# Performance work log

Hardware: AMD Instinct MI355X
Metric: run time of the kernel (lower is better)

## Reference

```python
import jax, jax.numpy as jnp
import numpy as np

EPS = 1e-7


def setup_inputs() -> dict:
    key = jax.random.key(0)
    k1, k2, k3, k4 = jax.random.split(key, 4)
    S, N, R, CIN, COUT = 16, 1024, 4, 128, 128
    A = jax.random.uniform(k1, (S, N, N, R + 1), dtype=jnp.float32)
    x = jax.random.normal(k2, (S, N, CIN), dtype=jnp.float32)
    weight = jax.random.normal(k3, (CIN, COUT, R), dtype=jnp.float32) * 0.02
    theta_root = jax.random.normal(k4, (CIN, COUT), dtype=jnp.float32) * 0.02
    return {"A": A, "x": x, "weight": weight, "theta_root": theta_root}


def reference(A, x, weight, theta_root):
    # Drop the last relation channel ('no-edge' type in MolGAN)
    Ar = A[..., :-1]                                   # (s, N, N, R)
    # Per-destination, per-relation degree normalization
    norm = 1.0 / (jnp.sum(Ar, axis=2) + EPS)           # (s, N, R)
    # Fused contraction: avoid materializing Theta_ij (s,N,N,in,out).
    # x_new[s,i,b] = sum_{j,c,a} A[s,i,j,c] * norm[s,i,c] * x[s,j,a] * W[a,b,c]
    m = jnp.einsum('sijc,sja->sica', Ar, x)            # (s, N, R, in)
    m = m * norm[..., None]                            # apply norm over (s,i,c)
    agg = jnp.einsum('sica,abc->sib', m, weight)       # (s, N, out)
    x_new = agg + x @ theta_root                       # root/self term
    return jnp.tanh(x_new)
```

## Files before the change

kernel.cpp:

```cpp
#include <hip/hip_runtime.h>
#include <hip/hip_bf16.h>
#include <math.h>

#define SS    16
#define NN    1024
#define RR    4
#define CINC  128
#define COUTC 128
#define RP1   5
#define EPSF  1e-7f

typedef __bf16 bf16x8 __attribute__((ext_vector_type(8)));
typedef __bf16 bf16x4 __attribute__((ext_vector_type(4)));
typedef float  f32x4  __attribute__((ext_vector_type(4)));

#define YT_BYTES ((size_t)SS * RR * COUTC * NN * 2)

__global__ __launch_bounds__(256) void convert_kernel(
    const float* __restrict__ weight, const float* __restrict__ theta,
    __bf16* __restrict__ wT)
{
    const int idx = blockIdx.x * 256 + threadIdx.x;
    const int a = idx >> 7, b = idx & 127;
    f32x4 wv = *(const f32x4*)(weight + ((size_t)a * COUTC + b) * RR);
    wT[(0 * COUTC + b) * CINC + a] = (__bf16)wv.x;
    wT[(1 * COUTC + b) * CINC + a] = (__bf16)wv.y;
    wT[(2 * COUTC + b) * CINC + a] = (__bf16)wv.z;
    wT[(3 * COUTC + b) * CINC + a] = (__bf16)wv.w;
    wT[(4 * COUTC + b) * CINC + a] = (__bf16)theta[(size_t)a * COUTC + b];
}

__global__ __launch_bounds__(256) void prep_kernel(
    const float* __restrict__ x, const __bf16* __restrict__ wT,
    __bf16* __restrict__ Yt)
{
    const int bx = blockIdx.x;
    const int s  = bx & 15;
    const int r  = bx >> 4;
    const int ch = r & 3;
    const int jt = r >> 2;

    const int t = threadIdx.x, lane = t & 63, w = t >> 6;
    const int m16 = lane & 15, quad = lane >> 4;

    const float*  xrow = x  + ((size_t)(s * NN) + jt * 64 + w * 16 + m16) * CINC;
    const __bf16* wch  = wT + (size_t)ch * COUTC * CINC;

    f32x4 acc[8];
#pragma unroll
    for (int i = 0; i < 8; ++i) acc[i] = (f32x4){0.f, 0.f, 0.f, 0.f};

#pragma unroll
    for (int k0 = 0; k0 < CINC; k0 += 32) {
        f32x4 xa = *(const f32x4*)(xrow + k0 + quad * 8);
        f32x4 xc = *(const f32x4*)(xrow + k0 + quad * 8 + 4);
        bf16x8 af;
        af[0] = (__bf16)xa.x; af[1] = (__bf16)xa.y; af[2] = (__bf16)xa.z; af[3] = (__bf16)xa.w;
        af[4] = (__bf16)xc.x; af[5] = (__bf16)xc.y; af[6] = (__bf16)xc.z; af[7] = (__bf16)xc.w;
#pragma unroll
        for (int bs = 0; bs < 8; ++bs) {
            const bf16x8 bf = *(const bf16x8*)(wch + (size_t)(bs * 16 + m16) * CINC + k0 + quad * 8);
            acc[bs] = __builtin_amdgcn_mfma_f32_16x16x32_bf16(af, bf, acc[bs], 0, 0, 0);
        }
    }

    const int j0 = jt * 64 + w * 16 + quad * 4;
#pragma unroll
    for (int bs = 0; bs < 8; ++bs) {
        const int b = bs * 16 + m16;
        bf16x4 v; v[0] = (__bf16)acc[bs][0]; v[1] = (__bf16)acc[bs][1];
                  v[2] = (__bf16)acc[bs][2]; v[3] = (__bf16)acc[bs][3];
        *(bf16x4*)(Yt + ((size_t)((s * 4 + ch) * COUTC + b)) * NN + j0) = v;
    }
}

__global__ __launch_bounds__(256, 4) void main_kernel(
    const float* __restrict__ A, const float* __restrict__ x,
    const __bf16* __restrict__ Yt, const __bf16* __restrict__ wT,
    float* __restrict__ out)
{
    const int bx = blockIdx.x;
    const int s  = bx & 15;
    const int i0 = (bx >> 4) * 16;

    __shared__ __bf16 lA[2][4][16][72];
    __shared__ float  lnorm[4][16];

    const int t = threadIdx.x;
    const int lane = t & 63, w = t >> 6;
    const int m16 = lane & 15, quad = lane >> 4;

    const int irow = t >> 4;
    const int q    = t & 15;

    const float* Ap = A + ((size_t)(s * NN + i0 + irow) * NN) * RP1 + q * 20;

    f32x4 accz[2];
    accz[0] = (f32x4){0.f, 0.f, 0.f, 0.f};
    accz[1] = (f32x4){0.f, 0.f, 0.f, 0.f};
    {
        const float*  xrow = x  + ((size_t)(s * NN) + i0 + m16) * CINC;
        const __bf16* wth  = wT + (size_t)4 * COUTC * CINC;
#pragma unroll
        for (int k0 = 0; k0 < CINC; k0 += 32) {
            f32x4 xa = *(const f32x4*)(xrow + k0 + quad * 8);
            f32x4 xc = *(const f32x4*)(xrow + k0 + quad * 8 + 4);
            bf16x8 af;
            af[0] = (__bf16)xa.x; af[1] = (__bf16)xa.y; af[2] = (__bf16)xa.z; af[3] = (__bf16)xa.w;
            af[4] = (__bf16)xc.x; af[5] = (__bf16)xc.y; af[6] = (__bf16)xc.z; af[7] = (__bf16)xc.w;
#pragma unroll
            for (int bs = 0; bs < 2; ++bs) {
                const bf16x8 bf = *(const bf16x8*)(wth + (size_t)(w * 32 + bs * 16 + m16) * CINC + k0 + quad * 8);
                accz[bs] = __builtin_amdgcn_mfma_f32_16x16x32_bf16(af, bf, accz[bs], 0, 0, 0);
            }
        }
    }

    float rs[4] = {0.f, 0.f, 0.f, 0.f};
    f32x4 acc[4][2];
#pragma unroll
    for (int c = 0; c < 4; ++c)
#pragma unroll
        for (int bs = 0; bs < 2; ++bs) acc[c][bs] = (f32x4){0.f, 0.f, 0.f, 0.f};

    const __bf16* Ys = Yt + (size_t)s * 4 * COUTC * NN;

    f32x4 ld[5];
#pragma unroll
    for (int u = 0; u < 5; ++u) ld[u] = __builtin_nontemporal_load((const f32x4*)Ap + u);

    for (int kk = 0; kk < 16; ++kk) {
        const int p = kk & 1;

        {
            const float v0[4] = {ld[0].x, ld[1].y, ld[2].z, ld[3].w};
            const float v1[4] = {ld[0].y, ld[1].z, ld[2].w, ld[4].x};
            const float v2[4] = {ld[0].z, ld[1].w, ld[3].x, ld[4].y};
            const float v3[4] = {ld[0].w, ld[2].x, ld[3].y, ld[4].z};
            const float* vv[4] = {v0, v1, v2, v3};
#pragma unroll
            for (int c = 0; c < 4; ++c) {
                const float* v = vv[c];
                rs[c] += v[0] + v[1] + v[2] + v[3];
                bf16x4 pk; pk[0] = (__bf16)v[0]; pk[1] = (__bf16)v[1];
                           pk[2] = (__bf16)v[2]; pk[3] = (__bf16)v[3];
                *(bf16x4*)&lA[p][c][irow][q * 4] = pk;
            }
        }
        __syncthreads();

        if (kk < 15) {
            Ap += 320;
#pragma unroll
            for (int u = 0; u < 5; ++u) ld[u] = __builtin_nontemporal_load((const f32x4*)Ap + u);
        }

#pragma unroll
        for (int c = 0; c < 4; ++c) {
            const __bf16* yp = Ys + (size_t)(c * COUTC + w * 32 + m16) * NN + kk * 64 + quad * 8;
#pragma unroll
            for (int ks = 0; ks < 2; ++ks) {
                const bf16x8 af = *(const bf16x8*)&lA[p][c][m16][ks * 32 + quad * 8];
                const bf16x8 b0 = *(const bf16x8*)(yp + ks * 32);
                const bf16x8 b1 = *(const bf16x8*)(yp + (size_t)16 * NN + ks * 32);
                acc[c][0] = __builtin_amdgcn_mfma_f32_16x16x32_bf16(af, b0, acc[c][0], 0, 0, 0);
                acc[c][1] = __builtin_amdgcn_mfma_f32_16x16x32_bf16(af, b1, acc[c][1], 0, 0, 0);
            }
        }
    }

#pragma unroll
    for (int c = 0; c < 4; ++c) {
        float v = rs[c];
        v += __shfl_xor(v, 1);
        v += __shfl_xor(v, 2);
        v += __shfl_xor(v, 4);
        v += __shfl_xor(v, 8);
        if (q == 0) lnorm[c][irow] = 1.0f / (v + EPSF);
    }
    __syncthreads();

    {
        f32x4 nv[4];
#pragma unroll
        for (int c = 0; c < 4; ++c) nv[c] = *(const f32x4*)&lnorm[c][quad * 4];
        const int row0 = i0 + quad * 4;
#pragma unroll
        for (int bs = 0; bs < 2; ++bs) {
            const int b = w * 32 + bs * 16 + m16;
#pragma unroll
            for (int r = 0; r < 4; ++r) {
                float v = acc[0][bs][r] * nv[0][r]
                        + acc[1][bs][r] * nv[1][r]
                        + acc[2][bs][r] * nv[2][r]
                        + acc[3][bs][r] * nv[3][r]
                        + accz[bs][r];
                out[((size_t)s * NN + row0 + r) * COUTC + b] = tanhf(v);
            }
        }
    }
}

extern "C" void kernel_launch(void* const* d_in, const int* in_sizes, int n_in,
                              void* d_out, int out_size, void* d_ws, size_t ws_size,
                              hipStream_t stream)
{
    const float* A      = (const float*)d_in[0];
    const float* x      = (const float*)d_in[1];
    const float* weight = (const float*)d_in[2];
    const float* theta  = (const float*)d_in[3];
    float* out = (float*)d_out;

    __bf16* Yt = (__bf16*)d_ws;
    __bf16* wT = (__bf16*)((char*)d_ws + YT_BYTES);

    convert_kernel<<<dim3(64), dim3(256), 0, stream>>>(weight, theta, wT);
    prep_kernel<<<dim3(SS * RR * 16), dim3(256), 0, stream>>>(x, wT, Yt);
    main_kernel<<<dim3(SS * 64), dim3(256), 0, stream>>>(A, x, Yt, wT, out);
}
```

Baseline: 608.1 us.

## Load adjacency directly into MFMA registers per wave, removing LDS staging

The main kernel no longer stages the A tile through double-buffered shared memory with block-wide barriers. Each wave now reads its 16x32x5 slice of A from global memory straight into registers, builds the bf16 MFMA A-operand there, and computes the row-sum normalization with wave shuffles. The change removes LDS traffic and __syncthreads, but all four waves now fetch the same A data, the explicit next-tile prefetch is gone, and the loads are no longer nontemporal. Launch bounds drop from 4 to 3 blocks per CU to allow more registers.

New measurement: 670.6 us. +10.3%, slower.

```diff
diff --git a/kernel.cpp b/kernel.cpp
--- a/kernel.cpp
+++ b/kernel.cpp
@@ -74,7 +74,7 @@
     }
 }
 
-__global__ __launch_bounds__(256, 4) void main_kernel(
+__global__ __launch_bounds__(256, 3) void main_kernel(
     const float* __restrict__ A, const float* __restrict__ x,
     const __bf16* __restrict__ Yt, const __bf16* __restrict__ wT,
     float* __restrict__ out)
@@ -83,17 +83,9 @@
     const int s  = bx & 15;
     const int i0 = (bx >> 4) * 16;
 
-    __shared__ __bf16 lA[2][4][16][72];
-    __shared__ float  lnorm[4][16];
-
     const int t = threadIdx.x;
     const int lane = t & 63, w = t >> 6;
     const int m16 = lane & 15, quad = lane >> 4;
-
-    const int irow = t >> 4;
-    const int q    = t & 15;
-
-    const float* Ap = A + ((size_t)(s * NN + i0 + irow) * NN) * RP1 + q * 20;
 
     f32x4 accz[2];
     accz[0] = (f32x4){0.f, 0.f, 0.f, 0.f};
@@ -124,79 +116,67 @@
         for (int bs = 0; bs < 2; ++bs) acc[c][bs] = (f32x4){0.f, 0.f, 0.f, 0.f};
 
     const __bf16* Ys = Yt + (size_t)s * 4 * COUTC * NN;
-
-    f32x4 ld[5];
-#pragma unroll
-    for (int u = 0; u < 5; ++u) ld[u] = __builtin_nontemporal_load((const f32x4*)Ap + u);
-
-    for (int kk = 0; kk < 16; ++kk) {
-        const int p = kk & 1;
-
-        {
-            const float v0[4] = {ld[0].x, ld[1].y, ld[2].z, ld[3].w};
-            const float v1[4] = {ld[0].y, ld[1].z, ld[2].w, ld[4].x};
-            const float v2[4] = {ld[0].z, ld[1].w, ld[3].x, ld[4].y};
-            const float v3[4] = {ld[0].w, ld[2].x, ld[3].y, ld[4].z};
-            const float* vv[4] = {v0, v1, v2, v3};
-#pragma unroll
-            for (int c = 0; c < 4; ++c) {
-                const float* v = vv[c];
-                rs[c] += v[0] + v[1] + v[2] + v[3];
-                bf16x4 pk; pk[0] = (__bf16)v[0]; pk[1] = (__bf16)v[1];
-                           pk[2] = (__bf16)v[2]; pk[3] = (__bf16)v[3];
-                *(bf16x4*)&lA[p][c][irow][q * 4] = pk;
+    const f32x4* Ap = (const f32x4*)(A + (((size_t)(s * NN + i0 + m16) * NN) + quad * 8) * RP1);
+
+    for (int kk = 0; kk < 32; ++kk) {
+        f32x4 ld[10];
+#pragma unroll
+        for (int u = 0; u < 10; ++u) ld[u] = Ap[u];
+
+        bf16x8 bfr[4][2];
+        const __bf16* yp = Ys + kk * 32 + quad * 8;
+#pragma unroll
+        for (int c = 0; c < 4; ++c)
+#pragma unroll
+            for (int bs = 0; bs < 2; ++bs)
+                bfr[c][bs] = *(const bf16x8*)(yp + (size_t)(c * COUTC + w * 32 + bs * 16 + m16) * NN);
+
+#pragma unroll
+        for (int c = 0; c < 4; ++c) {
+            bf16x8 af;
+            float sum = 0.f;
+#pragma unroll
+            for (int j = 0; j < 8; ++j) {
+                const int d = j * RP1 + c;
+                const float v = ld[d >> 2][d & 3];
+                sum += v;
+                af[j] = (__bf16)v;
             }
-        }
-        __syncthreads();
-
-        if (kk < 15) {
-            Ap += 320;
-#pragma unroll
-            for (int u = 0; u < 5; ++u) ld[u] = __builtin_nontemporal_load((const f32x4*)Ap + u);
-        }
-
-#pragma unroll
-        for (int c = 0; c < 4; ++c) {
-            const __bf16* yp = Ys + (size_t)(c * COUTC + w * 32 + m16) * NN + kk * 64 + quad * 8;
-#pragma unroll
-            for (int ks = 0; ks < 2; ++ks) {
-                const bf16x8 af = *(const bf16x8*)&lA[p][c][m16][ks * 32 + quad * 8];
-                const bf16x8 b0 = *(const bf16x8*)(yp + ks * 32);
-                const bf16x8 b1 = *(const bf16x8*)(yp + (size_t)16 * NN + ks * 32);
-                acc[c][0] = __builtin_amdgcn_mfma_f32_16x16x32_bf16(af, b0, acc[c][0], 0, 0, 0);
-                acc[c][1] = __builtin_amdgcn_mfma_f32_16x16x32_bf16(af, b1, acc[c][1], 0, 0, 0);
-            }
-        }
-    }
-
+            rs[c] += sum;
+            acc[c][0] = __builtin_amdgcn_mfma_f32_16x16x32_bf16(af, bfr[c][0], acc[c][0], 0, 0, 0);
+            acc[c][1] = __builtin_amdgcn_mfma_f32_16x16x32_bf16(af, bfr[c][1], acc[c][1], 0, 0, 0);
+        }
+
+        Ap += 40;
+    }
+
+    float nrm[4];
 #pragma unroll
     for (int c = 0; c < 4; ++c) {
         float v = rs[c];
-        v += __shfl_xor(v, 1);
-        v += __shfl_xor(v, 2);
-        v += __shfl_xor(v, 4);
-        v += __shfl_xor(v, 8);
-        if (q == 0) lnorm[c][irow] = 1.0f / (v + EPSF);
-    }
-    __syncthreads();
-
-    {
-        f32x4 nv[4];
-#pragma unroll
-        for (int c = 0; c < 4; ++c) nv[c] = *(const f32x4*)&lnorm[c][quad * 4];
-        const int row0 = i0 + quad * 4;
-#pragma unroll
-        for (int bs = 0; bs < 2; ++bs) {
-            const int b = w * 32 + bs * 16 + m16;
-#pragma unroll
-            for (int r = 0; r < 4; ++r) {
-                float v = acc[0][bs][r] * nv[0][r]
-                        + acc[1][bs][r] * nv[1][r]
-                        + acc[2][bs][r] * nv[2][r]
-                        + acc[3][bs][r] * nv[3][r]
-                        + accz[bs][r];
-                out[((size_t)s * NN + row0 + r) * COUTC + b] = tanhf(v);
-            }
+        v += __shfl_xor(v, 16);
+        v += __shfl_xor(v, 32);
+        nrm[c] = 1.0f / (v + EPSF);
+    }
+
+    float nr[4][4];
+#pragma unroll
+    for (int c = 0; c < 4; ++c)
+#pragma unroll
+        for (int r = 0; r < 4; ++r)
+            nr[c][r] = __shfl(nrm[c], quad * 4 + r);
+
+#pragma unroll
+    for (int bs = 0; bs < 2; ++bs) {
+        const int b = w * 32 + bs * 16 + m16;
+#pragma unroll
+        for (int r = 0; r < 4; ++r) {
+            float v = acc[0][bs][r] * nr[0][r]
+                    + acc[1][bs][r] * nr[1][r]
+                    + acc[2][bs][r] * nr[2][r]
+                    + acc[3][bs][r] * nr[3][r]
+                    + accz[bs][r];
+            out[((size_t)s * NN + i0 + quad * 4 + r) * COUTC + b] = tanhf(v);
         }
     }
 }
```
